# Kernel tuning notes

Hardware: AMD Instinct MI355X
Metric: run time of the kernel (lower is better)

The kernel has to match this reference:

```python
import jax, jax.numpy as jnp
import numpy as np

LEVEL_SHAPES = [(100, 134), (50, 67), (25, 34), (13, 17)]  # (H, W) per feature level
NH, NL, NP, D, DFF = 8, 4, 4, 256, 1024
DH = D // NH
LTOT = sum(h * w for h, w in LEVEL_SHAPES)  # 17821
BS, NQ = 4, 300


def _ln(x, w, b):
    m = x.mean(-1, keepdims=True)
    v = ((x - m) ** 2).mean(-1, keepdims=True)
    return (x - m) / jnp.sqrt(v + 1e-5) * w + b


def _mha(q, k, v, in_w, in_b, out_w, out_b):
    B, N, _ = q.shape
    wq, wk, wv = jnp.split(in_w, 3, axis=0)
    bq, bk, bv = jnp.split(in_b, 3)
    qh = (q @ wq.T + bq).reshape(B, N, NH, DH)
    kh = (k @ wk.T + bk).reshape(B, N, NH, DH)
    vh = (v @ wv.T + bv).reshape(B, N, NH, DH)
    a = jax.nn.softmax(jnp.einsum('bqhd,bkhd->bhqk', qh, kh) / float(np.sqrt(DH)), axis=-1)
    o = jnp.einsum('bhqk,bkhd->bqhd', a, vh).reshape(B, N, D)
    return o @ out_w.T + out_b


def _bilinear(img, grid):
    # img [B,C,H,W]; grid [B,N,2] in [-1,1]; align_corners=False, zero padding
    B, C, H, W = img.shape
    x = (grid[..., 0] + 1.0) * 0.5 * W - 0.5
    y = (grid[..., 1] + 1.0) * 0.5 * H - 0.5
    x0f = jnp.floor(x); y0f = jnp.floor(y)
    wx = x - x0f; wy = y - y0f
    x0 = x0f.astype(jnp.int32); y0 = y0f.astype(jnp.int32)
    flat = img.reshape(B, C, H * W)

    def gather(xi, yi):
        m = ((xi >= 0) & (xi < W) & (yi >= 0) & (yi < H)).astype(img.dtype)
        idx = jnp.clip(yi, 0, H - 1) * W + jnp.clip(xi, 0, W - 1)
        g = jnp.take_along_axis(flat, jnp.broadcast_to(idx[:, None, :], (B, C, idx.shape[-1])), axis=2)
        return g * m[:, None, :]

    return (gather(x0, y0) * ((1 - wx) * (1 - wy))[:, None]
            + gather(x0 + 1, y0) * (wx * (1 - wy))[:, None]
            + gather(x0, y0 + 1) * ((1 - wx) * wy)[:, None]
            + gather(x0 + 1, y0 + 1) * (wx * wy)[:, None])


def _msdeform(value, loc, aw):
    # value [B,L,NH,DH]; loc [B,Nq,NH,NL,NP,2] in [0,1]; aw [B,Nq,NH,NL,NP]
    B, Nq = loc.shape[0], loc.shape[1]
    outs = []
    start = 0
    for l, (Hl, Wl) in enumerate(LEVEL_SHAPES):
        v = value[:, start:start + Hl * Wl].transpose(0, 2, 3, 1).reshape(B * NH, DH, Hl, Wl)
        g = (2.0 * loc[:, :, :, l] - 1.0).transpose(0, 2, 1, 3, 4).reshape(B * NH, Nq * NP, 2)
        outs.append(_bilinear(v, g).reshape(B * NH, DH, Nq, NP))
        start += Hl * Wl
    samp = jnp.stack(outs, axis=3)  # [B*NH, DH, Nq, NL, NP]
    w = aw.transpose(0, 2, 1, 3, 4).reshape(B * NH, 1, Nq, NL, NP)
    out = (samp * w).sum(axis=(3, 4))  # [B*NH, DH, Nq]
    return out.reshape(B, NH, DH, Nq).transpose(0, 3, 1, 2).reshape(B, Nq, D)


def _deform_branch(q, ref, src_other, vw, vb, ow, ob, aww, awb, outw, outb):
    B, Nq, _ = q.shape
    value = (src_other @ vw.T + vb).reshape(B, -1, NH, DH)
    off = (q @ ow.T + ob).reshape(B, Nq, NH, NL, NP, 2)
    aw = jax.nn.softmax((q @ aww.T + awb).reshape(B, Nq, NH, NL * NP), axis=-1).reshape(B, Nq, NH, NL, NP)
    norm = jnp.array([[w, h] for h, w in LEVEL_SHAPES], dtype=q.dtype)  # (W,H) per level
    loc = ref[:, :, None, :, None, :] + off / norm[None, None, None, :, None, :]
    return _msdeform(value, loc, aw) @ outw.T + outb


def reference(tgt_RGB, tgt_T, query_pos_RGB, query_pos_T, ref_RGB, ref_T, src_RGB, src_T,
              sa_in_w, sa_in_b, sa_out_w, sa_out_b, ln_w, ln_b,
              ffn_w1, ffn_b1, ffn_w2, ffn_b2,
              val_w, val_b, off_w, off_b, aw_w, aw_b, cout_w, cout_b):
    # --- dual self-attention (eval mode: dropout = identity) ---
    q_RGB = tgt_RGB + query_pos_RGB
    q_T = tgt_T + query_pos_T
    sa_RGB = _mha(q_RGB, q_RGB, tgt_RGB, sa_in_w[0], sa_in_b[0], sa_out_w[0], sa_out_b[0])
    sa_T = _mha(q_T, q_T, tgt_T, sa_in_w[1], sa_in_b[1], sa_out_w[1], sa_out_b[1])
    tgt_RGB = _ln(tgt_RGB + sa_RGB, ln_w[0, 1], ln_b[0, 1])  # norm2_RGB
    tgt_T = _ln(tgt_T + sa_T, ln_w[1, 1], ln_b[1, 1])        # norm2_T
    # --- interactive multi-scale deformable cross-attn: RGB queries sample T memory & vice versa ---
    qc_RGB = tgt_RGB + query_pos_RGB
    qc_T = tgt_T + query_pos_T
    t2_RGB = _deform_branch(qc_RGB, ref_RGB, src_T, val_w[0], val_b[0], off_w[0], off_b[0], aw_w[0], aw_b[0], cout_w[0], cout_b[0])
    t2_T = _deform_branch(qc_T, ref_T, src_RGB, val_w[1], val_b[1], off_w[1], off_b[1], aw_w[1], aw_b[1], cout_w[1], cout_b[1])
    F_RGB, F_T = t2_RGB, t2_T
    # cross residuals exactly as in the torch layer (note the modality swap)
    r = tgt_T + t2_RGB
    t = r + t2_T
    tgt_RGB = _ln(r, ln_w[0, 0], ln_b[0, 0])  # norm1_RGB
    tgt_T = _ln(t, ln_w[1, 0], ln_b[1, 0])    # norm1_T
    # --- FFNs ---
    tgt_RGB = _ln(tgt_RGB + (jax.nn.relu(tgt_RGB @ ffn_w1[0].T + ffn_b1[0]) @ ffn_w2[0].T + ffn_b2[0]), ln_w[0, 2], ln_b[0, 2])
    tgt_T = _ln(tgt_T + (jax.nn.relu(tgt_T @ ffn_w1[1].T + ffn_b1[1]) @ ffn_w2[1].T + ffn_b2[1]), ln_w[1, 2], ln_b[1, 2])
    return tgt_RGB, tgt_T, F_RGB, F_T


def setup_inputs() -> dict:
    key = jax.random.key(0)
    ks = jax.random.split(key, 24)
    s = 0.05
    w = lambda k, shp: jax.random.normal(k, shp, dtype=jnp.float32) * s
    return {
        'tgt_RGB': jax.random.normal(ks[0], (BS, NQ, D), jnp.float32),
        'tgt_T': jax.random.normal(ks[1], (BS, NQ, D), jnp.float32),
        'query_pos_RGB': jax.random.normal(ks[2], (BS, NQ, D), jnp.float32),
        'query_pos_T': jax.random.normal(ks[3], (BS, NQ, D), jnp.float32),
        'ref_RGB': jax.random.uniform(ks[4], (BS, NQ, NL, 2), jnp.float32),
        'ref_T': jax.random.uniform(ks[5], (BS, NQ, NL, 2), jnp.float32),
        'src_RGB': jax.random.normal(ks[6], (BS, LTOT, D), jnp.float32),
        'src_T': jax.random.normal(ks[7], (BS, LTOT, D), jnp.float32),
        'sa_in_w': w(ks[8], (2, 3 * D, D)),
        'sa_in_b': jnp.zeros((2, 3 * D), jnp.float32),
        'sa_out_w': w(ks[9], (2, D, D)),
        'sa_out_b': jnp.zeros((2, D), jnp.float32),
        'ln_w': jnp.ones((2, 3, D), jnp.float32),
        'ln_b': jnp.zeros((2, 3, D), jnp.float32),
        'ffn_w1': w(ks[10], (2, DFF, D)),
        'ffn_b1': jnp.zeros((2, DFF), jnp.float32),
        'ffn_w2': w(ks[11], (2, D, DFF)),
        'ffn_b2': jnp.zeros((2, D), jnp.float32),
        'val_w': w(ks[12], (2, D, D)),
        'val_b': jnp.zeros((2, D), jnp.float32),
        'off_w': w(ks[13], (2, NH * NL * NP * 2, D)),
        'off_b': jax.random.normal(ks[14], (2, NH * NL * NP * 2), jnp.float32) * 0.5,
        'aw_w': w(ks[15], (2, NH * NL * NP, D)),
        'aw_b': jnp.zeros((2, NH * NL * NP), jnp.float32),
        'cout_w': w(ks[16], (2, D, D)),
        'cout_b': jnp.zeros((2, D), jnp.float32),
    }
```

## Files before the change

### kernel.cpp

```cpp
#include <hip/hip_runtime.h>
#include <cstddef>
#include <math.h>

#define NTOK 1200
#define LTOT_C 17821
#define MVAL 71284
#define STOK (NTOK * 256)

typedef __attribute__((ext_vector_type(8))) short bhalf8;
typedef __attribute__((ext_vector_type(4))) float f32x4;

static __device__ __forceinline__ short f2bf(float f) {
    unsigned u = __builtin_bit_cast(unsigned, f);
    u += 0x7fffu + ((u >> 16) & 1u);
    return (short)(u >> 16);
}
static __device__ __forceinline__ float bf2f(short s) {
    unsigned u = ((unsigned)(unsigned short)s) << 16;
    return __builtin_bit_cast(float, u);
}
static __device__ __forceinline__ bhalf8 cvt8(float4 a, float4 b) {
    bhalf8 h;
    h[0] = f2bf(a.x); h[1] = f2bf(a.y); h[2] = f2bf(a.z); h[3] = f2bf(a.w);
    h[4] = f2bf(b.x); h[5] = f2bf(b.y); h[6] = f2bf(b.z); h[7] = f2bf(b.w);
    return h;
}

struct WcvtArgs { const float* s[10]; short* d[10]; int n[10]; };
__global__ __launch_bounds__(256) void wcvt(WcvtArgs a) {
    const int ti = blockIdx.y;
    const float* s = a.s[ti];
    short* d = a.d[ti];
    const int n = a.n[ti];
    for (int base = (blockIdx.x * 256 + threadIdx.x) * 8; base < n; base += gridDim.x * 256 * 8) {
        const float4 f0 = *reinterpret_cast<const float4*>(s + base);
        const float4 f1 = *reinterpret_cast<const float4*>(s + base + 4);
        *reinterpret_cast<bhalf8*>(d + base) = cvt8(f0, f1);
    }
}

__global__ __launch_bounds__(256) void prep_act(
    const float* __restrict__ tgt0, const float* __restrict__ tgt1,
    const float* __restrict__ pos0, const float* __restrict__ pos1,
    short* __restrict__ qb_bf, short* __restrict__ tgtb,
    const float* __restrict__ off_b, const float* __restrict__ aw_b,
    float* __restrict__ baw)
{
    const int z = blockIdx.y;
    if (blockIdx.x == 0 && z == 0) {
        for (int i = threadIdx.x; i < 768; i += 256) {
            const int zz = i / 384, j = i - zz * 384;
            baw[i] = (j < 256) ? off_b[zz * 256 + j] : aw_b[zz * 128 + (j - 256)];
        }
    }
    const float* tg = z ? tgt1 : tgt0;
    const float* ps = z ? pos1 : pos0;
    const int base = (blockIdx.x * 256 + threadIdx.x) * 8;
    if (base >= STOK) return;
    const float4 t0 = *reinterpret_cast<const float4*>(tg + base);
    const float4 t1 = *reinterpret_cast<const float4*>(tg + base + 4);
    const float4 p0 = *reinterpret_cast<const float4*>(ps + base);
    const float4 p1 = *reinterpret_cast<const float4*>(ps + base + 4);
    float4 s0 = make_float4(t0.x + p0.x, t0.y + p0.y, t0.z + p0.z, t0.w + p0.w);
    float4 s1 = make_float4(t1.x + p1.x, t1.y + p1.y, t1.z + p1.z, t1.w + p1.w);
    *reinterpret_cast<bhalf8*>(qb_bf + (size_t)z * STOK + base) = cvt8(s0, s1);
    *reinterpret_cast<bhalf8*>(tgtb + (size_t)z * STOK + base) = cvt8(t0, t1);
}

template<bool A_FP32, bool HASRES, bool RELU, bool OUT_BF16, int BM>
__global__ __launch_bounds__(256) void gemm_bf16(
    const void* __restrict__ Av, const void* __restrict__ Av1, size_t aStrideZ, int lda,
    const short* __restrict__ Wv, size_t wStrideZ, int ldw,
    const float* __restrict__ bias, size_t biasStrideZ,
    const float* __restrict__ Res0, const float* __restrict__ Res1, int ldr,
    void* __restrict__ Cv, size_t cStrideZ, int ldc,
    int M, int K)
{
    constexpr int AIT = BM / 32;
    constexpr int MFR = BM / 32;
    __shared__ short As[BM * 64];
    __shared__ short Bs[128 * 64];
    const int z = blockIdx.z;
    const void* Asel = (Av1 != nullptr && z == 1) ? Av1 : Av;
    const size_t zoff = (Av1 != nullptr) ? 0 : (size_t)z * aStrideZ;
    const short* W = Wv + (size_t)z * wStrideZ;
    const float* bz = bias + (size_t)z * biasStrideZ;
    const int t = threadIdx.x;
    const int wave = t >> 6, lane = t & 63;
    const int l15 = lane & 15, l4 = lane >> 4;
    const int wr = wave >> 1, wc = wave & 1;
    const int bm = blockIdx.y * BM, bn = blockIdx.x * 128;
    f32x4 acc[MFR][4] = {};

    float4 paf[AIT][2];
    bhalf8 pab[AIT];
    bhalf8 pwb[4];
    const int NK = K >> 6;

    auto issue = [&](int k0) {
        #pragma unroll
        for (int i = 0; i < AIT; ++i) {
            const int G = t + i * 256;
            const int m = G >> 3, g = G & 7;
            const int row = bm + m;
            if (A_FP32) {
                if (row < M) {
                    const float* s = (const float*)Asel + zoff + (size_t)row * lda + k0 + g * 8;
                    paf[i][0] = *reinterpret_cast<const float4*>(s);
                    paf[i][1] = *reinterpret_cast<const float4*>(s + 4);
                } else {
                    paf[i][0] = make_float4(0.f, 0.f, 0.f, 0.f);
                    paf[i][1] = make_float4(0.f, 0.f, 0.f, 0.f);
                }
            } else {
                if (row < M) {
                    pab[i] = *reinterpret_cast<const bhalf8*>(
                        (const short*)Asel + zoff + (size_t)row * lda + k0 + g * 8);
                } else {
                    #pragma unroll
                    for (int q = 0; q < 8; ++q) pab[i][q] = 0;
                }
            }
        }
        #pragma unroll
        for (int i = 0; i < 4; ++i) {
            const int G = t + i * 256;
            const int n = G >> 3, g = G & 7;
            pwb[i] = *reinterpret_cast<const bhalf8*>(W + (size_t)(bn + n) * ldw + k0 + g * 8);
        }
    };
    auto commit = [&]() {
        #pragma unroll
        for (int i = 0; i < AIT; ++i) {
            const int G = t + i * 256;
            const int m = G >> 3, g = G & 7;
            bhalf8 h;
            if (A_FP32) h = cvt8(paf[i][0], paf[i][1]);
            else h = pab[i];
            *reinterpret_cast<bhalf8*>(&As[m * 64 + ((g ^ (m & 7)) << 3)]) = h;
        }
        #pragma unroll
        for (int i = 0; i < 4; ++i) {
            const int G = t + i * 256;
            const int n = G >> 3, g = G & 7;
            *reinterpret_cast<bhalf8*>(&Bs[n * 64 + ((g ^ (n & 7)) << 3)]) = pwb[i];
        }
    };
    auto compute = [&]() {
        #pragma unroll
        for (int kf = 0; kf < 2; ++kf) {
            bhalf8 af[MFR], bfv[4];
            #pragma unroll
            for (int mf = 0; mf < MFR; ++mf) {
                const int m = wr * (BM / 2) + (mf << 4) + l15;
                const int g = ((kf << 2) + l4) ^ (m & 7);
                af[mf] = *reinterpret_cast<const bhalf8*>(&As[m * 64 + (g << 3)]);
            }
            #pragma unroll
            for (int nf = 0; nf < 4; ++nf) {
                const int n = (wc << 6) + (nf << 4) + l15;
                const int g = ((kf << 2) + l4) ^ (n & 7);
                bfv[nf] = *reinterpret_cast<const bhalf8*>(&Bs[n * 64 + (g << 3)]);
            }
            #pragma unroll
            for (int mf = 0; mf < MFR; ++mf)
                #pragma unroll
                for (int nf = 0; nf < 4; ++nf)
                    acc[mf][nf] = __builtin_amdgcn_mfma_f32_16x16x32_bf16(
                        af[mf], bfv[nf], acc[mf][nf], 0, 0, 0);
        }
    };

    issue(0);
    commit();
    for (int ks = 0; ks < NK; ++ks) {
        __syncthreads();
        if (ks + 1 < NK) issue((ks + 1) << 6);
        compute();
        __syncthreads();
        if (ks + 1 < NK) commit();
    }

    const float* Rz = HASRES ? (z ? Res1 : Res0) : nullptr;
    float br[4];
    #pragma unroll
    for (int nf = 0; nf < 4; ++nf) br[nf] = bz[bn + (wc << 6) + (nf << 4) + l15];
    #pragma unroll
    for (int mf = 0; mf < MFR; ++mf) {
        #pragma unroll
        for (int j = 0; j < 4; ++j) {
            const int row = bm + wr * (BM / 2) + (mf << 4) + (l4 << 2) + j;
            if (row >= M) continue;
            const int colbase = bn + (wc << 6);
            #pragma unroll
            for (int nf = 0; nf < 4; ++nf) {
                const int col = colbase + (nf << 4) + l15;
                float v = acc[mf][nf][j] + br[nf];
                if (HASRES) v += Rz[(size_t)row * ldr + col];
                if (RELU) v = fmaxf(v, 0.f);
                if (OUT_BF16)
                    ((short*)Cv + (size_t)z * cStrideZ)[(size_t)row * ldc + col] = f2bf(v);
                else
                    ((float*)Cv + (size_t)z * cStrideZ)[(size_t)row * ldc + col] = v;
            }
        }
    }
}

__global__ __launch_bounds__(256) void attn2_kernel(
    const float* __restrict__ qkv_base, short* __restrict__ out_base)
{
    const float scale = 0.17677669529663687f;
    const float* qkv = qkv_base + (size_t)blockIdx.z * 921600;
    short* outp = out_base + (size_t)blockIdx.z * STOK;
    const int b = blockIdx.y >> 3, h = blockIdx.y & 7;
    const int t = threadIdx.x;
    const int ql = t & 31;
    const int kg = t >> 5;
    const int q = blockIdx.x * 32 + ql;
    const bool act = q < 300;
    const float* base = qkv + (size_t)b * 300 * 768;

    float qreg[32];
    if (act) {
        const float4* qp = reinterpret_cast<const float4*>(base + (size_t)q * 768 + h * 32);
        #pragma unroll
        for (int d4 = 0; d4 < 8; ++d4) {
            const float4 v = qp[d4];
            qreg[d4 * 4 + 0] = v.x; qreg[d4 * 4 + 1] = v.y;
            qreg[d4 * 4 + 2] = v.z; qreg[d4 * 4 + 3] = v.w;
        }
    }
    __shared__ float Ks[64][32];
    __shared__ float Vs[64][32];
    float m = -1e30f, l = 0.f, o[32];
    #pragma unroll
    for (int d = 0; d < 32; ++d) o[d] = 0.f;

    for (int k0 = 0; k0 < 300; k0 += 64) {
        const int cnt = min(64, 300 - k0);
        __syncthreads();
        for (int i = t; i < cnt * 32; i += 256) {
            const int kr = i >> 5, d = i & 31;
            Ks[kr][d] = base[(size_t)(k0 + kr) * 768 + 256 + h * 32 + d];
            Vs[kr][d] = base[(size_t)(k0 + kr) * 768 + 512 + h * 32 + d];
        }
        __syncthreads();
        if (act) {
            for (int kk = kg; kk < cnt; kk += 8) {
                const float4* krow = reinterpret_cast<const float4*>(&Ks[kk][0]);
                float s = 0.f;
                #pragma unroll
                for (int d4 = 0; d4 < 8; ++d4) {
                    const float4 kv = krow[d4];
                    s += qreg[d4 * 4 + 0] * kv.x + qreg[d4 * 4 + 1] * kv.y
                       + qreg[d4 * 4 + 2] * kv.z + qreg[d4 * 4 + 3] * kv.w;
                }
                s *= scale;
                const float4* vrow = reinterpret_cast<const float4*>(&Vs[kk][0]);
                if (s <= m) {
                    const float e = __expf(s - m);
                    l += e;
                    #pragma unroll
                    for (int d4 = 0; d4 < 8; ++d4) {
                        const float4 vv = vrow[d4];
                        o[d4 * 4 + 0] += e * vv.x; o[d4 * 4 + 1] += e * vv.y;
                        o[d4 * 4 + 2] += e * vv.z; o[d4 * 4 + 3] += e * vv.w;
                    }
                } else {
                    const float c = __expf(m - s);
                    l = l * c + 1.f;
                    #pragma unroll
                    for (int d4 = 0; d4 < 8; ++d4) {
                        const float4 vv = vrow[d4];
                        o[d4 * 4 + 0] = o[d4 * 4 + 0] * c + vv.x;
                        o[d4 * 4 + 1] = o[d4 * 4 + 1] * c + vv.y;
                        o[d4 * 4 + 2] = o[d4 * 4 + 2] * c + vv.z;
                        o[d4 * 4 + 3] = o[d4 * 4 + 3] * c + vv.w;
                    }
                    m = s;
                }
            }
        }
    }
    __shared__ float pm[32][8];
    __shared__ float pl[32][8];
    __shared__ float po[8][32][33];
    pm[ql][kg] = m; pl[ql][kg] = l;
    #pragma unroll
    for (int d = 0; d < 32; ++d) po[kg][d][ql] = o[d];
    __syncthreads();
    if (kg == 0) {
        float M = pm[ql][0];
        #pragma unroll
        for (int i = 1; i < 8; ++i) M = fmaxf(M, pm[ql][i]);
        float L = 0.f;
        #pragma unroll
        for (int i = 0; i < 8; ++i) L += pl[ql][i] * __expf(pm[ql][i] - M);
        const float invL = 1.f / L;
        #pragma unroll
        for (int i = 0; i < 8; ++i) pm[ql][i] = __expf(pm[ql][i] - M) * invL;
    }
    __syncthreads();
    if (act) {
        #pragma unroll
        for (int dd = 0; dd < 4; ++dd) {
            const int d = kg * 4 + dd;
            float v = 0.f;
            #pragma unroll
            for (int i = 0; i < 8; ++i) v += pm[ql][i] * po[i][d][ql];
            outp[((size_t)b * 300 + q) * 256 + h * 32 + d] = f2bf(v);
        }
    }
}

#define LN_BODY(vexpr, widx)                                                  \
    const int row = blockIdx.x, t = threadIdx.x, z = blockIdx.y;              \
    (void)z;                                                                  \
    const int i = row * 256 + t;                                              \
    const float v = (vexpr);                                                  \
    __shared__ float r1[4], r2[4];                                            \
    float s = v;                                                              \
    _Pragma("unroll")                                                         \
    for (int o = 32; o; o >>= 1) s += __shfl_xor(s, o);                       \
    if ((t & 63) == 0) r1[t >> 6] = s;                                        \
    __syncthreads();                                                          \
    const float mean = (r1[0] + r1[1] + r1[2] + r1[3]) * (1.f / 256.f);       \
    const float dd = v - mean;                                                \
    float sq = dd * dd;                                                       \
    _Pragma("unroll")                                                         \
    for (int o = 32; o; o >>= 1) sq += __shfl_xor(sq, o);                     \
    if ((t & 63) == 0) r2[t >> 6] = sq;                                       \
    __syncthreads();                                                          \
    const float var = (r2[0] + r2[1] + r2[2] + r2[3]) * (1.f / 256.f);        \
    const float y = dd * rsqrtf(var + 1e-5f) * ln_w[(widx) * 256 + t]         \
                    + ln_b[(widx) * 256 + t];

__global__ __launch_bounds__(256) void ln2_fused(
    const float* __restrict__ presum, const float* __restrict__ pos0,
    const float* __restrict__ pos1, const float* __restrict__ ln_w,
    const float* __restrict__ ln_b, short* __restrict__ qc_bf,
    float* __restrict__ tgt2T)
{
    LN_BODY(presum[(size_t)z * STOK + i], z * 3 + 1)
    const float* pos = z ? pos1 : pos0;
    qc_bf[(size_t)z * STOK + i] = f2bf(y + pos[i]);
    if (z == 1) tgt2T[i] = y;
}

__global__ __launch_bounds__(256) void ln1_fused(
    const float* __restrict__ tgt2T, const float* __restrict__ out2,
    const float* __restrict__ out3, const float* __restrict__ ln_w,
    const float* __restrict__ ln_b, short* __restrict__ ln1b,
    float* __restrict__ ln1f)
{
    LN_BODY(tgt2T[row * 256 + t] + out2[row * 256 + t] + (z ? out3[row * 256 + t] : 0.f), z * 3 + 0)
    ln1b[(size_t)z * STOK + i] = f2bf(y);
    ln1f[(size_t)z * STOK + i] = y;
}

__global__ __launch_bounds__(256) void ln3_kernel(
    const float* __restrict__ ffny, const float* __restrict__ ln_w,
    const float* __restrict__ ln_b, float* __restrict__ o0,
    float* __restrict__ o1)
{
    LN_BODY(ffny[(size_t)z * STOK + i], z * 3 + 2)
    (z ? o1 : o0)[i] = y;
}

__global__ __launch_bounds__(256) void sample_kernel(
    const short* __restrict__ valb, const float* __restrict__ oaw,
    const float* __restrict__ ref0, const float* __restrict__ ref1,
    short* __restrict__ out)
{
    const int HL[4] = {100, 50, 25, 13};
    const int WL[4] = {134, 67, 34, 17};
    const int ST[4] = {0, 13400, 16750, 17600};
    const int z = blockIdx.y;
    const int t = threadIdx.x;
    const int wave = t >> 6, lane = t & 63;
    const int qi = wave >> 1, hh = wave & 1;
    const int pp = lane >> 5, h4 = (lane >> 3) & 3, dl = lane & 7;
    const int h = hh * 4 + h4;
    const int bq = blockIdx.x * 2 + qi;
    const int b = bq / 300;
    const float* op = oaw + ((size_t)z * NTOK + bq) * 384;
    const float* offp = op + h * 32;
    const float* awp  = op + 256 + h * 16;
    const float* refp = (z ? ref1 : ref0) + (size_t)bq * 8;
    const short* vb = valb + (size_t)z * MVAL * 256 + (size_t)b * LTOT_C * 256;
    const int co = h * 32 + dl * 4;

    float w16[16];
    float mx = -1e30f;
    #pragma unroll
    for (int i = 0; i < 16; ++i) { w16[i] = awp[i]; mx = fmaxf(mx, w16[i]); }
    float ssum = 0.f;
    #pragma unroll
    for (int i = 0; i < 16; ++i) { w16[i] = __expf(w16[i] - mx); ssum += w16[i]; }
    const float sinv = 1.f / ssum;

    float a0 = 0.f, a1 = 0.f, a2 = 0.f, a3 = 0.f;
#define TAP(cond, ridx, wv)                                                   \
    if (cond) {                                                               \
        const short4 sv = *reinterpret_cast<const short4*>(                   \
            vb + (size_t)(ridx) * 256 + co);                                  \
        a0 += (wv) * bf2f(sv.x); a1 += (wv) * bf2f(sv.y);                     \
        a2 += (wv) * bf2f(sv.z); a3 += (wv) * bf2f(sv.w);                     \
    }
    #pragma unroll
    for (int l = 0; l < 4; ++l) {
        const int Wl = WL[l], Hl = HL[l];
        const float rx = refp[l * 2] * (float)Wl - 0.5f;
        const float ry = refp[l * 2 + 1] * (float)Hl - 0.5f;
        #pragma unroll
        for (int j = 0; j < 2; ++j) {
            const int p = pp * 2 + j;
            const float px = rx + offp[(l * 4 + p) * 2];
            const float py = ry + offp[(l * 4 + p) * 2 + 1];
            const float wgt = w16[l * 4 + p] * sinv;
            const float x0f = floorf(px), y0f = floorf(py);
            const float wx = px - x0f, wy = py - y0f;
            const int x0 = (int)x0f, y0 = (int)y0f;
            const bool xa = (x0 >= 0) & (x0 < Wl);
            const bool xb = (x0 >= -1) & (x0 < Wl - 1);
            const bool ya = (y0 >= 0) & (y0 < Hl);
            const bool yb = (y0 >= -1) & (y0 < Hl - 1);
            const int rbase = ST[l] + y0 * Wl + x0;
            const float w00 = wgt * (1.f - wx) * (1.f - wy);
            const float w10 = wgt * wx * (1.f - wy);
            const float w01 = wgt * (1.f - wx) * wy;
            const float w11 = wgt * wx * wy;
            TAP(ya & xa, rbase, w00)
            TAP(ya & xb, rbase + 1, w10)
            TAP(yb & xa, rbase + Wl, w01)
            TAP(yb & xb, rbase + Wl + 1, w11)
        }
    }
#undef TAP
    a0 += __shfl_xor(a0, 32);
    a1 += __shfl_xor(a1, 32);
    a2 += __shfl_xor(a2, 32);
    a3 += __shfl_xor(a3, 32);
    if (pp == 0) {
        short4 o;
        o.x = f2bf(a0); o.y = f2bf(a1); o.z = f2bf(a2); o.w = f2bf(a3);
        *reinterpret_cast<short4*>(&out[((size_t)z * NTOK + bq) * 256 + co]) = o;
    }
}

extern "C" void kernel_launch(void* const* d_in, const int* in_sizes, int n_in,
                              void* d_out, int out_size, void* d_ws, size_t ws_size,
                              hipStream_t stream) {
    const float* tgt[2] = {(const float*)d_in[0], (const float*)d_in[1]};
    const float* pos[2] = {(const float*)d_in[2], (const float*)d_in[3]};
    const float* ref[2] = {(const float*)d_in[4], (const float*)d_in[5]};
    const float* src[2] = {(const float*)d_in[6], (const float*)d_in[7]};
    const float* sa_in_w  = (const float*)d_in[8];
    const float* sa_in_b  = (const float*)d_in[9];
    const float* sa_out_w = (const float*)d_in[10];
    const float* sa_out_b = (const float*)d_in[11];
    const float* ln_w = (const float*)d_in[12];
    const float* ln_b = (const float*)d_in[13];
    const float* ffn_w1 = (const float*)d_in[14];
    const float* ffn_b1 = (const float*)d_in[15];
    const float* ffn_w2 = (const float*)d_in[16];
    const float* ffn_b2 = (const float*)d_in[17];
    const float* val_w = (const float*)d_in[18];
    const float* val_b = (const float*)d_in[19];
    const float* off_w = (const float*)d_in[20];
    const float* off_b = (const float*)d_in[21];
    const float* aw_w = (const float*)d_in[22];
    const float* aw_b = (const float*)d_in[23];
    const float* cout_w = (const float*)d_in[24];
    const float* cout_b = (const float*)d_in[25];

    char* base = (char*)d_ws;
    size_t off = 0;
    auto alloc = [&](size_t bytes) -> char* {
        char* p = base + off;
        off += (bytes + 255) & ~(size_t)255;
        return p;
    };
    short* wbf   = (short*)alloc((size_t)2031616 * 2);
    float* baw   = (float*)alloc(768 * 4);
    short* qb_bf = (short*)alloc((size_t)2 * STOK * 2);
    short* tgtb  = (short*)alloc((size_t)2 * STOK * 2);
    float* qkv   = (float*)alloc((size_t)2 * 921600 * 4);
    short* attno = (short*)alloc((size_t)2 * STOK * 2);
    float* presum= (float*)alloc((size_t)2 * STOK * 4);
    short* qc_bf = (short*)alloc((size_t)2 * STOK * 2);
    float* tgt2T = (float*)alloc((size_t)STOK * 4);
    float* oawb  = (float*)alloc((size_t)2 * NTOK * 384 * 4);
    short* valb  = (short*)alloc((size_t)2 * MVAL * 256 * 2);
    short* samp  = (short*)alloc((size_t)2 * STOK * 2);
    short* ln1b  = (short*)alloc((size_t)2 * STOK * 2);
    float* ln1f  = (float*)alloc((size_t)2 * STOK * 4);
    short* ffnh  = (short*)alloc((size_t)2 * NTOK * 1024 * 2);
    float* ffny  = (float*)alloc((size_t)2 * STOK * 4);

    short* sa_in_bf  = wbf + 0;
    short* sa_out_bf = wbf + 393216;
    short* ffn1_bf   = wbf + 524288;
    short* ffn2_bf   = wbf + 1048576;
    short* val_bf    = wbf + 1572864;
    short* cout_bf   = wbf + 1703936;
    short* oaw_bf    = wbf + 1835008;

    float* out0 = (float*)d_out;
    float* out1 = out0 + STOK;
    float* out2 = out1 + STOK;
    float* out3 = out2 + STOK;

    const dim3 b256(256);

    WcvtArgs wa;
    wa.s[0] = sa_in_w;        wa.d[0] = sa_in_bf;       wa.n[0] = 393216;
    wa.s[1] = sa_out_w;       wa.d[1] = sa_out_bf;      wa.n[1] = 131072;
    wa.s[2] = ffn_w1;         wa.d[2] = ffn1_bf;        wa.n[2] = 524288;
    wa.s[3] = ffn_w2;         wa.d[3] = ffn2_bf;        wa.n[3] = 524288;
    wa.s[4] = val_w;          wa.d[4] = val_bf;         wa.n[4] = 131072;
    wa.s[5] = cout_w;         wa.d[5] = cout_bf;        wa.n[5] = 131072;
    wa.s[6] = off_w;          wa.d[6] = oaw_bf;         wa.n[6] = 65536;
    wa.s[7] = aw_w;           wa.d[7] = oaw_bf + 65536; wa.n[7] = 32768;
    wa.s[8] = off_w + 65536;  wa.d[8] = oaw_bf + 98304; wa.n[8] = 65536;
    wa.s[9] = aw_w + 32768;   wa.d[9] = oaw_bf + 163840;wa.n[9] = 32768;
    wcvt<<<dim3(128, 10), b256, 0, stream>>>(wa);

    prep_act<<<dim3(150, 2), b256, 0, stream>>>(tgt[0], tgt[1], pos[0], pos[1],
                                                qb_bf, tgtb, off_b, aw_b, baw);

    gemm_bf16<true, false, false, true, 128><<<dim3(2, 557, 2), b256, 0, stream>>>(
        src[1], src[0], 0, 256, val_bf, 65536, 256, val_b, 256, nullptr, nullptr, 0,
        valb, (size_t)MVAL * 256, 256, MVAL, 256);

    gemm_bf16<false, false, false, false, 64><<<dim3(4, 19, 2), b256, 0, stream>>>(
        qb_bf, nullptr, (size_t)STOK, 256, sa_in_bf, 196608, 256, sa_in_b, 768,
        nullptr, nullptr, 0, qkv, 921600, 768, NTOK, 256);
    gemm_bf16<false, false, false, false, 64><<<dim3(2, 19, 2), b256, 0, stream>>>(
        tgtb, nullptr, (size_t)STOK, 256, sa_in_bf + 512 * 256, 196608, 256, sa_in_b + 512, 768,
        nullptr, nullptr, 0, qkv + 512, 921600, 768, NTOK, 256);

    attn2_kernel<<<dim3(10, 32, 2), b256, 0, stream>>>(qkv, attno);

    gemm_bf16<false, true, false, false, 64><<<dim3(2, 19, 2), b256, 0, stream>>>(
        attno, nullptr, (size_t)STOK, 256, sa_out_bf, 65536, 256, sa_out_b, 256,
        tgt[0], tgt[1], 256, presum, (size_t)STOK, 256, NTOK, 256);

    ln2_fused<<<dim3(NTOK, 2), b256, 0, stream>>>(presum, pos[0], pos[1], ln_w, ln_b, qc_bf, tgt2T);

    gemm_bf16<false, false, false, false, 64><<<dim3(3, 19, 2), b256, 0, stream>>>(
        qc_bf, nullptr, (size_t)STOK, 256, oaw_bf, 98304, 256, baw, 384,
        nullptr, nullptr, 0, oawb, (size_t)NTOK * 384, 384, NTOK, 256);

    sample_kernel<<<dim3(600, 2), b256, 0, stream>>>(valb, oawb, ref[0], ref[1], samp);

    gemm_bf16<false, false, false, false, 64><<<dim3(2, 19, 2), b256, 0, stream>>>(
        samp, nullptr, (size_t)STOK, 256, cout_bf, 65536, 256, cout_b, 256,
        nullptr, nullptr, 0, out2, (size_t)STOK, 256, NTOK, 256);

    ln1_fused<<<dim3(NTOK, 2), b256, 0, stream>>>(tgt2T, out2, out3, ln_w, ln_b, ln1b, ln1f);

    gemm_bf16<false, false, true, true, 64><<<dim3(8, 19, 2), b256, 0, stream>>>(
        ln1b, nullptr, (size_t)STOK, 256, ffn1_bf, 262144, 256, ffn_b1, 1024,
        nullptr, nullptr, 0, ffnh, (size_t)NTOK * 1024, 1024, NTOK, 256);

    gemm_bf16<false, true, false, false, 64><<<dim3(2, 19, 2), b256, 0, stream>>>(
        ffnh, nullptr, (size_t)NTOK * 1024, 1024, ffn2_bf, 262144, 1024, ffn_b2, 256,
        ln1f, ln1f + STOK, 256, ffny, (size_t)STOK, 256, NTOK, 1024);

    ln3_kernel<<<dim3(NTOK, 2), b256, 0, stream>>>(ffny, ln_w, ln_b, out0, out1);
}
```

Baseline: 213.7 us.

## Prefetch two K-tiles ahead in GEMM with compile-time K loop count

The GEMM kernel now holds two register staging slots, so global loads for tile k+2 are issued while tile k is computed and tile k+1 waits in registers. The K-loop trip count becomes a template parameter, which lets the loop fully unroll so the slot indices resolve at compile time, and sched_barriers keep the loads from being reordered. The aim is to hide global-memory latency in the mostly small, latency-bound GEMMs. The cost is about double the staging registers, which may lower occupancy, especially for the fp32-A BM=128 value projection.

```diff
diff --git a/kernel.cpp b/kernel.cpp
--- a/kernel.cpp
+++ b/kernel.cpp
@@ -67,14 +67,14 @@
     *reinterpret_cast<bhalf8*>(tgtb + (size_t)z * STOK + base) = cvt8(t0, t1);
 }
 
-template<bool A_FP32, bool HASRES, bool RELU, bool OUT_BF16, int BM>
+template<bool A_FP32, bool HASRES, bool RELU, bool OUT_BF16, int BM, int NK>
 __global__ __launch_bounds__(256) void gemm_bf16(
     const void* __restrict__ Av, const void* __restrict__ Av1, size_t aStrideZ, int lda,
     const short* __restrict__ Wv, size_t wStrideZ, int ldw,
     const float* __restrict__ bias, size_t biasStrideZ,
     const float* __restrict__ Res0, const float* __restrict__ Res1, int ldr,
     void* __restrict__ Cv, size_t cStrideZ, int ldc,
-    int M, int K)
+    int M)
 {
     constexpr int AIT = BM / 32;
     constexpr int MFR = BM / 32;
@@ -92,12 +92,11 @@
     const int bm = blockIdx.y * BM, bn = blockIdx.x * 128;
     f32x4 acc[MFR][4] = {};
 
-    float4 paf[AIT][2];
-    bhalf8 pab[AIT];
-    bhalf8 pwb[4];
-    const int NK = K >> 6;
-
-    auto issue = [&](int k0) {
+    float4 paf[2][AIT][2];
+    bhalf8 pab[2][AIT];
+    bhalf8 pwb[2][4];
+
+    auto issue = [&](int slot, int k0) {
         #pragma unroll
         for (int i = 0; i < AIT; ++i) {
             const int G = t + i * 256;
@@ -106,19 +105,19 @@
             if (A_FP32) {
                 if (row < M) {
                     const float* s = (const float*)Asel + zoff + (size_t)row * lda + k0 + g * 8;
-                    paf[i][0] = *reinterpret_cast<const float4*>(s);
-                    paf[i][1] = *reinterpret_cast<const float4*>(s + 4);
+                    paf[slot][i][0] = *reinterpret_cast<const float4*>(s);
+                    paf[slot][i][1] = *reinterpret_cast<const float4*>(s + 4);
                 } else {
-                    paf[i][0] = make_float4(0.f, 0.f, 0.f, 0.f);
-                    paf[i][1] = make_float4(0.f, 0.f, 0.f, 0.f);
+                    paf[slot][i][0] = make_float4(0.f, 0.f, 0.f, 0.f);
+                    paf[slot][i][1] = make_float4(0.f, 0.f, 0.f, 0.f);
                 }
             } else {
                 if (row < M) {
-                    pab[i] = *reinterpret_cast<const bhalf8*>(
+                    pab[slot][i] = *reinterpret_cast<const bhalf8*>(
                         (const short*)Asel + zoff + (size_t)row * lda + k0 + g * 8);
                 } else {
                     #pragma unroll
-                    for (int q = 0; q < 8; ++q) pab[i][q] = 0;
+                    for (int q = 0; q < 8; ++q) pab[slot][i][q] = 0;
                 }
             }
         }
@@ -126,24 +125,24 @@
         for (int i = 0; i < 4; ++i) {
             const int G = t + i * 256;
             const int n = G >> 3, g = G & 7;
-            pwb[i] = *reinterpret_cast<const bhalf8*>(W + (size_t)(bn + n) * ldw + k0 + g * 8);
+            pwb[slot][i] = *reinterpret_cast<const bhalf8*>(W + (size_t)(bn + n) * ldw + k0 + g * 8);
         }
     };
-    auto commit = [&]() {
+    auto commit = [&](int slot) {
         #pragma unroll
         for (int i = 0; i < AIT; ++i) {
             const int G = t + i * 256;
             const int m = G >> 3, g = G & 7;
             bhalf8 h;
-            if (A_FP32) h = cvt8(paf[i][0], paf[i][1]);
-            else h = pab[i];
+            if (A_FP32) h = cvt8(paf[slot][i][0], paf[slot][i][1]);
+            else h = pab[slot][i];
             *reinterpret_cast<bhalf8*>(&As[m * 64 + ((g ^ (m & 7)) << 3)]) = h;
         }
         #pragma unroll
         for (int i = 0; i < 4; ++i) {
             const int G = t + i * 256;
             const int n = G >> 3, g = G & 7;
-            *reinterpret_cast<bhalf8*>(&Bs[n * 64 + ((g ^ (n & 7)) << 3)]) = pwb[i];
+            *reinterpret_cast<bhalf8*>(&Bs[n * 64 + ((g ^ (n & 7)) << 3)]) = pwb[slot][i];
         }
     };
     auto compute = [&]() {
@@ -171,14 +170,18 @@
         }
     };
 
-    issue(0);
-    commit();
+    issue(0, 0);
+    issue(1, 64);
+    __builtin_amdgcn_sched_barrier(0);
+    commit(0);
+    #pragma unroll
     for (int ks = 0; ks < NK; ++ks) {
         __syncthreads();
-        if (ks + 1 < NK) issue((ks + 1) << 6);
+        if (ks + 2 < NK) issue(ks & 1, (ks + 2) << 6);
+        __builtin_amdgcn_sched_barrier(0);
         compute();
         __syncthreads();
-        if (ks + 1 < NK) commit();
+        if (ks + 1 < NK) commit((ks + 1) & 1);
     }
 
     const float* Rz = HASRES ? (z ? Res1 : Res0) : nullptr;
@@ -530,44 +533,44 @@
     prep_act<<<dim3(150, 2), b256, 0, stream>>>(tgt[0], tgt[1], pos[0], pos[1],
                                                 qb_bf, tgtb, off_b, aw_b, baw);
 
-    gemm_bf16<true, false, false, true, 128><<<dim3(2, 557, 2), b256, 0, stream>>>(
+    gemm_bf16<true, false, false, true, 128, 4><<<dim3(2, 557, 2), b256, 0, stream>>>(
         src[1], src[0], 0, 256, val_bf, 65536, 256, val_b, 256, nullptr, nullptr, 0,
-        valb, (size_t)MVAL * 256, 256, MVAL, 256);
-
-    gemm_bf16<false, false, false, false, 64><<<dim3(4, 19, 2), b256, 0, stream>>>(
+        valb, (size_t)MVAL * 256, 256, MVAL);
+
+    gemm_bf16<false, false, false, false, 64, 4><<<dim3(4, 19, 2), b256, 0, stream>>>(
         qb_bf, nullptr, (size_t)STOK, 256, sa_in_bf, 196608, 256, sa_in_b, 768,
-        nullptr, nullptr, 0, qkv, 921600, 768, NTOK, 256);
-    gemm_bf16<false, false, false, false, 64><<<dim3(2, 19, 2), b256, 0, stream>>>(
+        nullptr, nullptr, 0, qkv, 921600, 768, NTOK);
+    gemm_bf16<false, false, false, false, 64, 4><<<dim3(2, 19, 2), b256, 0, stream>>>(
         tgtb, nullptr, (size_t)STOK, 256, sa_in_bf + 512 * 256, 196608, 256, sa_in_b + 512, 768,
-        nullptr, nullptr, 0, qkv + 512, 921600, 768, NTOK, 256);
+        nullptr, nullptr, 0, qkv + 512, 921600, 768, NTOK);
 
     attn2_kernel<<<dim3(10, 32, 2), b256, 0, stream>>>(qkv, attno);
 
-    gemm_bf16<false, true, false, false, 64><<<dim3(2, 19, 2), b256, 0, stream>>>(
+    gemm_bf16<false, true, false, false, 64, 4><<<dim3(2, 19, 2), b256, 0, stream>>>(
         attno, nullptr, (size_t)STOK, 256, sa_out_bf, 65536, 256, sa_out_b, 256,
-        tgt[0], tgt[1], 256, presum, (size_t)STOK, 256, NTOK, 256);
+        tgt[0], tgt[1], 256, presum, (size_t)STOK, 256, NTOK);
 
     ln2_fused<<<dim3(NTOK, 2), b256, 0, stream>>>(presum, pos[0], pos[1], ln_w, ln_b, qc_bf, tgt2T);
 
-    gemm_bf16<false, false, false, false, 64><<<dim3(3, 19, 2), b256, 0, stream>>>(
+    gemm_bf16<false, false, false, false, 64, 4><<<dim3(3, 19, 2), b256, 0, stream>>>(
         qc_bf, nullptr, (size_t)STOK, 256, oaw_bf, 98304, 256, baw, 384,
-        nullptr, nullptr, 0, oawb, (size_t)NTOK * 384, 384, NTOK, 256);
+        nullptr, nullptr, 0, oawb, (size_t)NTOK * 384, 384, NTOK);
 
     sample_kernel<<<dim3(600, 2), b256, 0, stream>>>(valb, oawb, ref[0], ref[1], samp);
 
-    gemm_bf16<false, false, false, false, 64><<<dim3(2, 19, 2), b256, 0, stream>>>(
+    gemm_bf16<false, false, false, false, 64, 4><<<dim3(2, 19, 2), b256, 0, stream>>>(
         samp, nullptr, (size_t)STOK, 256, cout_bf, 65536, 256, cout_b, 256,
-        nullptr, nullptr, 0, out2, (size_t)STOK, 256, NTOK, 256);
+        nullptr, nullptr, 0, out2, (size_t)STOK, 256, NTOK);
 
     ln1_fused<<<dim3(NTOK, 2), b256, 0, stream>>>(tgt2T, out2, out3, ln_w, ln_b, ln1b, ln1f);
 
-    gemm_bf16<false, false, true, true, 64><<<dim3(8, 19, 2), b256, 0, stream>>>(
+    gemm_bf16<false, false, true, true, 64, 4><<<dim3(8, 19, 2), b256, 0, stream>>>(
         ln1b, nullptr, (size_t)STOK, 256, ffn1_bf, 262144, 256, ffn_b1, 1024,
-        nullptr, nullptr, 0, ffnh, (size_t)NTOK * 1024, 1024, NTOK, 256);
-
-    gemm_bf16<false, true, false, false, 64><<<dim3(2, 19, 2), b256, 0, stream>>>(
+        nullptr, nullptr, 0, ffnh, (size_t)NTOK * 1024, 1024, NTOK);
+
+    gemm_bf16<false, true, false, false, 64, 16><<<dim3(2, 19, 2), b256, 0, stream>>>(
         ffnh, nullptr, (size_t)NTOK * 1024, 1024, ffn2_bf, 262144, 1024, ffn_b2, 256,
-        ln1f, ln1f + STOK, 256, ffny, (size_t)STOK, 256, NTOK, 1024);
+        ln1f, ln1f + STOK, 256, ffny, (size_t)STOK, 256, NTOK);
 
     ln3_kernel<<<dim3(NTOK, 2), b256, 0, stream>>>(ffny, ln_w, ln_b, out0, out1);
 }
```

New measurement: 208.4 us. 2.5% less time.
